# Kernel optimization log

Hardware: AMD Instinct MI355X
Metric: run time of the kernel (lower is better)

## Reference

```python
import jax, jax.numpy as jnp
import numpy as np

B, C, D, H, W = 1, 64, 24, 24, 24
N = D * H * W
K = D + H + W - 2  # cross neighbors per node (self deduped)
DS, GD = 64, 64    # d_sim, g_dim
GROUPS = C // 4
EPS = 1e-5
N_ITERS = 2        # pool_strides = [1, 1]


def _build_nbr_idx():
    i, j, k = np.meshgrid(np.arange(D), np.arange(H), np.arange(W), indexing='ij')
    i, j, k = i.reshape(-1), j.reshape(-1), k.reshape(-1)
    a0 = (j * W + k)[:, None] + np.arange(D)[None, :] * (H * W)      # (N, D) full depth line (incl self)
    full1 = (i * H * W + k)[:, None] + np.arange(H)[None, :] * W     # (N, H)
    a1 = full1[np.arange(H)[None, :] != j[:, None]].reshape(N, H - 1)
    full2 = (i * H * W + j * W)[:, None] + np.arange(W)[None, :]     # (N, W)
    a2 = full2[np.arange(W)[None, :] != k[:, None]].reshape(N, W - 1)
    return np.concatenate([a0, a1, a2], axis=1).astype(np.int32)     # (N, K)


def setup_inputs() -> dict:
    key = jax.random.key(0)
    ks = jax.random.split(key, 8)
    s = 0.05
    return {
        'x': jax.random.normal(ks[0], (B, C, D, H, W), jnp.float32),
        'nbr_idx': jnp.asarray(_build_nbr_idx()),
        'phi_w': jax.random.normal(ks[1], (DS, C), jnp.float32) * s,
        'phi_b': jnp.zeros((DS,), jnp.float32),
        'theta_w': jax.random.normal(ks[2], (DS, C), jnp.float32) * s,
        'theta_b': jnp.zeros((DS,), jnp.float32),
        'G_w': jax.random.normal(ks[3], (GD, C), jnp.float32) * s,
        'G_b': jnp.zeros((GD,), jnp.float32),
        'r_w': jax.random.normal(ks[4], (C, GD), jnp.float32) * s,
        'r_b': jnp.zeros((C,), jnp.float32),
        'gn_gamma': jnp.ones((N_ITERS, C), jnp.float32),
        'gn_beta': jnp.zeros((N_ITERS, C), jnp.float32),
        'bn_gamma': jnp.ones((C,), jnp.float32),
        'bn_beta': jnp.zeros((C,), jnp.float32),
        'bn_mean': jnp.zeros((C,), jnp.float32),
        'bn_var': jnp.ones((C,), jnp.float32),
    }


def _group_norm(v, gamma, beta):
    vg = v.reshape(B, GROUPS, C // GROUPS, D, H, W)
    m = vg.mean(axis=(2, 3, 4, 5), keepdims=True)
    var = ((vg - m) ** 2).mean(axis=(2, 3, 4, 5), keepdims=True)
    vn = ((vg - m) / jnp.sqrt(var + EPS)).reshape(B, C, D, H, W)
    return vn * gamma[None, :, None, None, None] + beta[None, :, None, None, None]


def reference(x, nbr_idx, phi_w, phi_b, theta_w, theta_b, G_w, G_b, r_w, r_b,
              gn_gamma, gn_beta, bn_gamma, bn_beta, bn_mean, bn_var):
    h = x
    for it in range(N_ITERS):
        hf = h.reshape(B, C, N).transpose(2, 0, 1)                    # (N, B, C) node features
        theta = jnp.einsum('nbc,dc->nbd', hf, theta_w) + theta_b     # (N, B, DS) queries
        phi_all = jnp.einsum('nbc,dc->nbd', hf, phi_w) + phi_b       # (N, B, DS) keys (pre-gather)
        g_all = jnp.einsum('nbc,gc->nbg', hf, G_w) + G_b             # (N, B, GD) values (pre-gather)
        phi_e = phi_all[nbr_idx]                                      # (N, K, B, DS) mailbox gather
        g_e = g_all[nbr_idx]                                          # (N, K, B, GD)
        f = jnp.einsum('nbd,nkbd->nbk', theta, phi_e)                # attention logits over K
        a = jax.nn.softmax(f, axis=-1)                                # non_local_merge 'softmax'
        y = jnp.einsum('nbk,nkbg->nbg', a, g_e)                      # weighted value sum
        cross = jnp.einsum('nbg,cg->nbc', y, r_w) + r_b              # (N, B, C) output proj
        cross = cross.transpose(1, 2, 0).reshape(B, C, D, H, W)
        h = h + _group_norm(cross, gn_gamma[it], gn_beta[it])
    # BatchNorm3d (eval, running stats) + ReLU
    bc = lambda v: v[None, :, None, None, None]
    out = (h - bc(bn_mean)) / jnp.sqrt(bc(bn_var) + EPS) * bc(bn_gamma) + bc(bn_beta)
    return jax.nn.relu(out)
```

## Files before the change

### kernel.cpp

```cpp
#include <hip/hip_runtime.h>
#include <math.h>

#define NN 13824
#define LW 24

__global__ __launch_bounds__(256) void apply_proj_kernel(
    const float* __restrict__ x,
    const float* __restrict__ cross, const float* __restrict__ gsum,
    const float* __restrict__ gn_g, const float* __restrict__ gn_b,
    float* __restrict__ h_out, int mode,
    const float* __restrict__ theta_w, const float* __restrict__ theta_b,
    const float* __restrict__ phi_w, const float* __restrict__ phi_b,
    const float* __restrict__ g_w, const float* __restrict__ g_b,
    float* __restrict__ theta, float* __restrict__ phi, float* __restrict__ gv)
{
    __shared__ float hs[64 * 64];
    __shared__ float ws[64 * 68];

    const int tid = threadIdx.x;
    const int tile = blockIdx.x / 3, ts = blockIdx.x % 3;
    const int n0 = tile * 64;

    const float* wsel = (ts == 0) ? theta_w : (ts == 1) ? phi_w : g_w;
    const float* bsel = (ts == 0) ? theta_b : (ts == 1) ? phi_b : g_b;
    float*       osel = (ts == 0) ? theta   : (ts == 1) ? phi   : gv;

    if (mode == 0) {
        for (int i = tid; i < 4096; i += 256) {
            int c = i >> 6, nl = i & 63;
            hs[c * 64 + nl] = x[(size_t)c * NN + n0 + nl];
        }
    } else {
        for (int i = tid; i < 4096; i += 256) {
            int nl = i >> 6, c = i & 63;
            ws[c * 68 + nl] = cross[(size_t)(n0 + nl) * 64 + c];
        }
        __syncthreads();
        const float inv_cnt = 1.f / 55296.f;
        for (int i = tid; i < 4096; i += 256) {
            int c = i >> 6, nl = i & 63;
            int gr = c >> 2;
            float mean = gsum[gr * 16] * inv_cnt;
            float var = gsum[512 + gr * 16] * inv_cnt - mean * mean;
            float v = (ws[c * 68 + nl] - mean) * rsqrtf(var + 1e-5f) * gn_g[c] + gn_b[c];
            size_t o = (size_t)c * NN + n0 + nl;
            float hv = x[o] + v;
            hs[c * 64 + nl] = hv;
            if (ts == 0) h_out[o] = hv;
        }
        __syncthreads();
    }

    for (int i = tid; i < 4096; i += 256) {
        int d = i >> 6, c = i & 63;
        ws[c * 68 + d] = wsel[d * 64 + c];
    }
    __syncthreads();

    const int d0  = (tid & 15) * 4;
    const int nl0 = (tid >> 4) * 4;
    float acc[4][4];
    #pragma unroll
    for (int q = 0; q < 4; q++)
        #pragma unroll
        for (int j = 0; j < 4; j++) acc[q][j] = 0.f;

    #pragma unroll 4
    for (int c = 0; c < 64; c++) {
        float4 hv = *(const float4*)&hs[c * 64 + nl0];
        float4 wv = *(const float4*)&ws[c * 68 + d0];
        #pragma unroll
        for (int j = 0; j < 4; j++) {
            float w = (&wv.x)[j];
            acc[0][j] += hv.x * w;
            acc[1][j] += hv.y * w;
            acc[2][j] += hv.z * w;
            acc[3][j] += hv.w * w;
        }
    }
    float4 bias = *(const float4*)&bsel[d0];
    #pragma unroll
    for (int q = 0; q < 4; q++) {
        float4 v;
        v.x = acc[q][0] + bias.x; v.y = acc[q][1] + bias.y;
        v.z = acc[q][2] + bias.z; v.w = acc[q][3] + bias.w;
        *(float4*)&osel[(size_t)(n0 + nl0 + q) * 64 + d0] = v;
    }
}

__global__ __launch_bounds__(128) void line_attn_kernel(
    const float* __restrict__ theta,
    const float* __restrict__ phi,
    const float* __restrict__ gv,
    float* __restrict__ y_part,
    float* __restrict__ l_part,
    float* __restrict__ gsum)
{
    __shared__ float th[2][LW * 68], ph[2][LW * 68], gs[2][LW * 68];
    __shared__ float P[2][LW * 28];

    const int tid = threadIdx.x;
    const int wv = tid >> 6, lane = tid & 63;
    const int gl = blockIdx.x * 2 + wv;
    const int axis = gl / 576, L = gl % 576;

    if (blockIdx.x == 0) {
        for (int i = tid; i < 1024; i += 128) gsum[i] = 0.f;
    }

    int base, stride;
    if (axis == 0)      { base = L * 24;                    stride = 1;   }
    else if (axis == 1) { base = (L / 24) * 576 + (L % 24); stride = 24;  }
    else                { base = L;                         stride = 576; }
    const bool excl = (axis != 2);

    #pragma unroll
    for (int q = 0; q < 6; q++) {
        int idx = q * 64 + lane;
        int row = idx >> 4, c4 = (idx & 15) * 4;
        size_t g = (size_t)(base + row * stride) * 64 + c4;
        int la = row * 68 + c4;
        *(float4*)&th[wv][la] = *(const float4*)&theta[g];
        *(float4*)&ph[wv][la] = *(const float4*)&phi[g];
        *(float4*)&gs[wv][la] = *(const float4*)&gv[g];
    }

    const int r0 = (lane >> 3) * 3, c0 = (lane & 7) * 3;
    float sa[3][3];
    #pragma unroll
    for (int a = 0; a < 3; a++)
        #pragma unroll
        for (int b = 0; b < 3; b++) sa[a][b] = 0.f;

    #pragma unroll 4
    for (int d4 = 0; d4 < 64; d4 += 4) {
        float4 t[3], p[3];
        #pragma unroll
        for (int a = 0; a < 3; a++) t[a] = *(const float4*)&th[wv][(r0 + a) * 68 + d4];
        #pragma unroll
        for (int b = 0; b < 3; b++) p[b] = *(const float4*)&ph[wv][(c0 + b) * 68 + d4];
        #pragma unroll
        for (int a = 0; a < 3; a++)
            #pragma unroll
            for (int b = 0; b < 3; b++)
                sa[a][b] += t[a].x * p[b].x + t[a].y * p[b].y +
                            t[a].z * p[b].z + t[a].w * p[b].w;
    }
    #pragma unroll
    for (int a = 0; a < 3; a++)
        #pragma unroll
        for (int b = 0; b < 3; b++) {
            float e = (excl && (r0 + a) == (c0 + b)) ? 0.f : __expf(sa[a][b]);
            P[wv][(r0 + a) * 28 + c0 + b] = e;
        }

    if (lane < 24) {
        float s = 0.f;
        #pragma unroll
        for (int c4 = 0; c4 < 24; c4 += 4) {
            float4 pv = *(const float4*)&P[wv][lane * 28 + c4];
            s += pv.x + pv.y + pv.z + pv.w;
        }
        l_part[(size_t)axis * NN + base + lane * stride] = s;
    }

    float acc[24];
    #pragma unroll
    for (int r = 0; r < 24; r++) acc[r] = 0.f;
    #pragma unroll
    for (int c4 = 0; c4 < 24; c4 += 4) {
        float g0 = gs[wv][(c4 + 0) * 68 + lane];
        float g1 = gs[wv][(c4 + 1) * 68 + lane];
        float g2 = gs[wv][(c4 + 2) * 68 + lane];
        float g3 = gs[wv][(c4 + 3) * 68 + lane];
        #pragma unroll
        for (int r = 0; r < 24; r++) {
            float4 pv = *(const float4*)&P[wv][r * 28 + c4];
            acc[r] += pv.x * g0 + pv.y * g1 + pv.z * g2 + pv.w * g3;
        }
    }
    float* yp = y_part + (size_t)axis * NN * 64;
    #pragma unroll
    for (int r = 0; r < 24; r++)
        yp[(size_t)(base + r * stride) * 64 + lane] = acc[r];
}

__global__ __launch_bounds__(256) void combine_kernel(
    const float* __restrict__ y_part, const float* __restrict__ l_part,
    const float* __restrict__ r_w, const float* __restrict__ r_b,
    float* __restrict__ cross, float* __restrict__ gsum)
{
    __shared__ float ys[16 * 68];
    __shared__ float red_s[4][64], red_ss[4][64];

    const int tid = threadIdx.x;
    const int d = tid & 63, w = tid >> 6;
    const int n0 = blockIdx.x * 16;
    const size_t S = (size_t)NN * 64;

    #pragma unroll
    for (int q = 0; q < 4; q++) {
        int nn = w * 4 + q;
        int n = n0 + nn;
        float lv = l_part[n] + l_part[NN + n] + l_part[2 * NN + n];
        size_t o = (size_t)n * 64 + d;
        float yv = y_part[o] + y_part[S + o] + y_part[2 * S + o];
        ys[nn * 68 + d] = yv / lv;
    }
    __syncthreads();

    const int c = d;
    float rb = r_b[c];
    float acc[4] = {rb, rb, rb, rb};
    for (int dd = 0; dd < 64; dd += 4) {
        float4 r4 = *(const float4*)&r_w[c * 64 + dd];
        #pragma unroll
        for (int q = 0; q < 4; q++) {
            float4 y4 = *(const float4*)&ys[(w * 4 + q) * 68 + dd];
            acc[q] += r4.x * y4.x + r4.y * y4.y + r4.z * y4.z + r4.w * y4.w;
        }
    }
    float s = 0.f, ss = 0.f;
    #pragma unroll
    for (int q = 0; q < 4; q++) {
        int n = n0 + w * 4 + q;
        cross[(size_t)n * 64 + c] = acc[q];
        s += acc[q];
        ss += acc[q] * acc[q];
    }
    red_s[w][c] = s;
    red_ss[w][c] = ss;
    __syncthreads();
    if (w == 0) {
        float ts  = red_s[0][c] + red_s[1][c] + red_s[2][c] + red_s[3][c];
        float tss = red_ss[0][c] + red_ss[1][c] + red_ss[2][c] + red_ss[3][c];
        ts  += __shfl_xor(ts, 1);  ts  += __shfl_xor(ts, 2);
        tss += __shfl_xor(tss, 1); tss += __shfl_xor(tss, 2);
        if ((c & 3) == 0) {
            atomicAdd(&gsum[(c >> 2) * 16], ts);
            atomicAdd(&gsum[512 + (c >> 2) * 16], tss);
        }
    }
}

__global__ __launch_bounds__(256) void final_kernel(
    const float* __restrict__ cross,
    const float* __restrict__ gsum,
    const float* __restrict__ gn_g, const float* __restrict__ gn_b,
    const float* __restrict__ h_in,
    const float* __restrict__ bn_g, const float* __restrict__ bn_b,
    const float* __restrict__ bn_m, const float* __restrict__ bn_v,
    float* __restrict__ out)
{
    __shared__ float t[64 * 65];
    const int tid = threadIdx.x;
    const int n0 = blockIdx.x * 64;
    for (int i = tid; i < 4096; i += 256) {
        int nl = i >> 6, c = i & 63;
        t[c * 65 + nl] = cross[(size_t)(n0 + nl) * 64 + c];
    }
    __syncthreads();
    const float inv_cnt = 1.f / 55296.f;
    for (int i = tid; i < 4096; i += 256) {
        int c = i >> 6, nl = i & 63;
        int gr = c >> 2;
        float mean = gsum[gr * 16] * inv_cnt;
        float var = gsum[512 + gr * 16] * inv_cnt - mean * mean;
        float v = (t[c * 65 + nl] - mean) * rsqrtf(var + 1e-5f) * gn_g[c] + gn_b[c];
        size_t o = (size_t)c * NN + n0 + nl;
        float h2 = h_in[o] + v;
        float bnv = (h2 - bn_m[c]) * rsqrtf(bn_v[c] + 1e-5f) * bn_g[c] + bn_b[c];
        out[o] = fmaxf(bnv, 0.f);
    }
}

extern "C" void kernel_launch(void* const* d_in, const int* in_sizes, int n_in,
                              void* d_out, int out_size, void* d_ws, size_t ws_size,
                              hipStream_t stream)
{
    const float* x        = (const float*)d_in[0];
    const float* phi_w    = (const float*)d_in[2];
    const float* phi_b    = (const float*)d_in[3];
    const float* theta_w  = (const float*)d_in[4];
    const float* theta_b  = (const float*)d_in[5];
    const float* G_w      = (const float*)d_in[6];
    const float* G_b      = (const float*)d_in[7];
    const float* r_w      = (const float*)d_in[8];
    const float* r_b      = (const float*)d_in[9];
    const float* gn_gamma = (const float*)d_in[10];
    const float* gn_beta  = (const float*)d_in[11];
    const float* bn_gamma = (const float*)d_in[12];
    const float* bn_beta  = (const float*)d_in[13];
    const float* bn_mean  = (const float*)d_in[14];
    const float* bn_var   = (const float*)d_in[15];

    float* ws = (float*)d_ws;
    const size_t S = (size_t)NN * 64;
    float* h1    = ws;
    float* theta = ws + S;
    float* phi   = ws + 2 * S;
    float* gv    = ws + 3 * S;
    float* ypart = ws + 4 * S;
    float* cross = ws + 7 * S;
    float* lpart = ws + 8 * S;
    float* gsum  = ws + 8 * S + 3 * NN;

    apply_proj_kernel<<<648, 256, 0, stream>>>(x, cross, gsum, gn_gamma, gn_beta,
                                               h1, 0,
                                               theta_w, theta_b, phi_w, phi_b,
                                               G_w, G_b, theta, phi, gv);
    line_attn_kernel<<<864, 128, 0, stream>>>(theta, phi, gv, ypart, lpart, gsum);
    combine_kernel<<<864, 256, 0, stream>>>(ypart, lpart, r_w, r_b, cross, gsum);
    apply_proj_kernel<<<648, 256, 0, stream>>>(x, cross, gsum, gn_gamma, gn_beta,
                                               h1, 1,
                                               theta_w, theta_b, phi_w, phi_b,
                                               G_w, G_b, theta, phi, gv);
    line_attn_kernel<<<864, 128, 0, stream>>>(theta, phi, gv, ypart, lpart, gsum);
    combine_kernel<<<864, 256, 0, stream>>>(ypart, lpart, r_w, r_b, cross, gsum);
    final_kernel<<<216, 256, 0, stream>>>(cross, gsum, gn_gamma + 64, gn_beta + 64,
                                          h1, bn_gamma, bn_beta, bn_mean, bn_var,
                                          (float*)d_out);
}
```

Baseline: 224.0 us.

## Fuse all stages into one persistent kernel with grid-wide barriers

Replaces the seven separate launches (projection, line attention, combine twice, then final) with one persistent kernel of 512 blocks. The blocks loop over work units in each phase and sync between phases with an atomic-counter grid barrier. This removes per-launch overhead and the idle tails between kernels. The attention phase now packs four lines per block and reads the value vectors straight from global memory instead of staging them in LDS, which frees shared memory. The risks are that all blocks must be co-resident or the barrier deadlocks, that barrier spin costs are added, and that the value reads become uncoalesced, strided global loads.

```diff
diff --git a/kernel.cpp b/kernel.cpp
--- a/kernel.cpp
+++ b/kernel.cpp
@@ -3,110 +3,130 @@
 
 #define NN 13824
 #define LW 24
-
-__global__ __launch_bounds__(256) void apply_proj_kernel(
-    const float* __restrict__ x,
-    const float* __restrict__ cross, const float* __restrict__ gsum,
-    const float* __restrict__ gn_g, const float* __restrict__ gn_b,
-    float* __restrict__ h_out, int mode,
+#define GRID 512
+#define NTHR 256
+
+__device__ __forceinline__ void gbar(unsigned* cnt, unsigned* gen)
+{
+    __syncthreads();
+    if (threadIdx.x == 0) {
+        __threadfence();
+        unsigned g = __hip_atomic_load(gen, __ATOMIC_RELAXED, __HIP_MEMORY_SCOPE_AGENT);
+        unsigned a = __hip_atomic_fetch_add(cnt, 1u, __ATOMIC_ACQ_REL, __HIP_MEMORY_SCOPE_AGENT);
+        if (a == (unsigned)gridDim.x - 1u) {
+            __hip_atomic_store(cnt, 0u, __ATOMIC_RELAXED, __HIP_MEMORY_SCOPE_AGENT);
+            __hip_atomic_store(gen, g + 1u, __ATOMIC_RELEASE, __HIP_MEMORY_SCOPE_AGENT);
+        } else {
+            while (__hip_atomic_load(gen, __ATOMIC_RELAXED, __HIP_MEMORY_SCOPE_AGENT) == g)
+                __builtin_amdgcn_s_sleep(2);
+            __builtin_amdgcn_fence(__ATOMIC_ACQUIRE, "agent");
+        }
+    }
+    __syncthreads();
+}
+
+__device__ void proj_phase(float* __restrict__ smem,
+    const float* __restrict__ x, const float* __restrict__ cross,
+    const float* __restrict__ gsum, const float* __restrict__ gn_g,
+    const float* __restrict__ gn_b, float* __restrict__ h_out, int mode,
     const float* __restrict__ theta_w, const float* __restrict__ theta_b,
     const float* __restrict__ phi_w, const float* __restrict__ phi_b,
     const float* __restrict__ g_w, const float* __restrict__ g_b,
     float* __restrict__ theta, float* __restrict__ phi, float* __restrict__ gv)
 {
-    __shared__ float hs[64 * 64];
-    __shared__ float ws[64 * 68];
-
+    float* hs = smem;
+    float* ws = smem + 4096;
     const int tid = threadIdx.x;
-    const int tile = blockIdx.x / 3, ts = blockIdx.x % 3;
-    const int n0 = tile * 64;
-
-    const float* wsel = (ts == 0) ? theta_w : (ts == 1) ? phi_w : g_w;
-    const float* bsel = (ts == 0) ? theta_b : (ts == 1) ? phi_b : g_b;
-    float*       osel = (ts == 0) ? theta   : (ts == 1) ? phi   : gv;
-
-    if (mode == 0) {
-        for (int i = tid; i < 4096; i += 256) {
-            int c = i >> 6, nl = i & 63;
-            hs[c * 64 + nl] = x[(size_t)c * NN + n0 + nl];
-        }
-    } else {
-        for (int i = tid; i < 4096; i += 256) {
-            int nl = i >> 6, c = i & 63;
-            ws[c * 68 + nl] = cross[(size_t)(n0 + nl) * 64 + c];
-        }
-        __syncthreads();
-        const float inv_cnt = 1.f / 55296.f;
-        for (int i = tid; i < 4096; i += 256) {
-            int c = i >> 6, nl = i & 63;
-            int gr = c >> 2;
-            float mean = gsum[gr * 16] * inv_cnt;
-            float var = gsum[512 + gr * 16] * inv_cnt - mean * mean;
-            float v = (ws[c * 68 + nl] - mean) * rsqrtf(var + 1e-5f) * gn_g[c] + gn_b[c];
-            size_t o = (size_t)c * NN + n0 + nl;
-            float hv = x[o] + v;
-            hs[c * 64 + nl] = hv;
-            if (ts == 0) h_out[o] = hv;
-        }
-        __syncthreads();
-    }
-
-    for (int i = tid; i < 4096; i += 256) {
-        int d = i >> 6, c = i & 63;
-        ws[c * 68 + d] = wsel[d * 64 + c];
-    }
-    __syncthreads();
-
-    const int d0  = (tid & 15) * 4;
-    const int nl0 = (tid >> 4) * 4;
-    float acc[4][4];
-    #pragma unroll
-    for (int q = 0; q < 4; q++)
-        #pragma unroll
-        for (int j = 0; j < 4; j++) acc[q][j] = 0.f;
-
-    #pragma unroll 4
-    for (int c = 0; c < 64; c++) {
-        float4 hv = *(const float4*)&hs[c * 64 + nl0];
-        float4 wv = *(const float4*)&ws[c * 68 + d0];
-        #pragma unroll
-        for (int j = 0; j < 4; j++) {
-            float w = (&wv.x)[j];
-            acc[0][j] += hv.x * w;
-            acc[1][j] += hv.y * w;
-            acc[2][j] += hv.z * w;
-            acc[3][j] += hv.w * w;
-        }
-    }
-    float4 bias = *(const float4*)&bsel[d0];
-    #pragma unroll
-    for (int q = 0; q < 4; q++) {
-        float4 v;
-        v.x = acc[q][0] + bias.x; v.y = acc[q][1] + bias.y;
-        v.z = acc[q][2] + bias.z; v.w = acc[q][3] + bias.w;
-        *(float4*)&osel[(size_t)(n0 + nl0 + q) * 64 + d0] = v;
-    }
-}
-
-__global__ __launch_bounds__(128) void line_attn_kernel(
-    const float* __restrict__ theta,
-    const float* __restrict__ phi,
-    const float* __restrict__ gv,
-    float* __restrict__ y_part,
-    float* __restrict__ l_part,
-    float* __restrict__ gsum)
-{
-    __shared__ float th[2][LW * 68], ph[2][LW * 68], gs[2][LW * 68];
-    __shared__ float P[2][LW * 28];
-
+
+    for (int unit = blockIdx.x; unit < 648; unit += GRID) {
+        const int tile = unit / 3, ts = unit % 3;
+        const int n0 = tile * 64;
+        const float* wsel = (ts == 0) ? theta_w : (ts == 1) ? phi_w : g_w;
+        const float* bsel = (ts == 0) ? theta_b : (ts == 1) ? phi_b : g_b;
+        float*       osel = (ts == 0) ? theta   : (ts == 1) ? phi   : gv;
+
+        if (mode == 0) {
+            for (int i = tid; i < 4096; i += NTHR) {
+                int c = i >> 6, nl = i & 63;
+                hs[c * 64 + nl] = x[(size_t)c * NN + n0 + nl];
+            }
+        } else {
+            for (int i = tid; i < 4096; i += NTHR) {
+                int nl = i >> 6, c = i & 63;
+                ws[c * 68 + nl] = cross[(size_t)(n0 + nl) * 64 + c];
+            }
+            __syncthreads();
+            const float inv_cnt = 1.f / 55296.f;
+            for (int i = tid; i < 4096; i += NTHR) {
+                int c = i >> 6, nl = i & 63;
+                int gr = c >> 2;
+                float mean = gsum[gr * 16] * inv_cnt;
+                float var = gsum[512 + gr * 16] * inv_cnt - mean * mean;
+                float v = (ws[c * 68 + nl] - mean) * rsqrtf(var + 1e-5f) * gn_g[c] + gn_b[c];
+                size_t o = (size_t)c * NN + n0 + nl;
+                float hv = x[o] + v;
+                hs[c * 64 + nl] = hv;
+                if (ts == 0) h_out[o] = hv;
+            }
+            __syncthreads();
+        }
+
+        for (int i = tid; i < 4096; i += NTHR) {
+            int d = i >> 6, c = i & 63;
+            ws[c * 68 + d] = wsel[d * 64 + c];
+        }
+        __syncthreads();
+
+        const int d0  = (tid & 15) * 4;
+        const int nl0 = (tid >> 4) * 4;
+        float acc[4][4];
+        #pragma unroll
+        for (int q = 0; q < 4; q++)
+            #pragma unroll
+            for (int j = 0; j < 4; j++) acc[q][j] = 0.f;
+
+        #pragma unroll 4
+        for (int c = 0; c < 64; c++) {
+            float4 hv = *(const float4*)&hs[c * 64 + nl0];
+            float4 wv = *(const float4*)&ws[c * 68 + d0];
+            #pragma unroll
+            for (int j = 0; j < 4; j++) {
+                float w = (&wv.x)[j];
+                acc[0][j] += hv.x * w;
+                acc[1][j] += hv.y * w;
+                acc[2][j] += hv.z * w;
+                acc[3][j] += hv.w * w;
+            }
+        }
+        float4 bias = *(const float4*)&bsel[d0];
+        #pragma unroll
+        for (int q = 0; q < 4; q++) {
+            float4 v;
+            v.x = acc[q][0] + bias.x; v.y = acc[q][1] + bias.y;
+            v.z = acc[q][2] + bias.z; v.w = acc[q][3] + bias.w;
+            *(float4*)&osel[(size_t)(n0 + nl0 + q) * 64 + d0] = v;
+        }
+        __syncthreads();
+    }
+}
+
+__device__ void attn_phase(float* __restrict__ smem,
+    const float* __restrict__ theta, const float* __restrict__ phi,
+    const float* __restrict__ gv, float* __restrict__ y_part,
+    float* __restrict__ l_part, float* __restrict__ gsum)
+{
     const int tid = threadIdx.x;
+    if (blockIdx.x == 0) {
+        for (int i = tid; i < 1024; i += NTHR) gsum[i] = 0.f;
+    }
     const int wv = tid >> 6, lane = tid & 63;
-    const int gl = blockIdx.x * 2 + wv;
+    const int gl = blockIdx.x * 4 + wv;
+    if (gl >= 1728) return;
     const int axis = gl / 576, L = gl % 576;
 
-    if (blockIdx.x == 0) {
-        for (int i = tid; i < 1024; i += 128) gsum[i] = 0.f;
-    }
+    float* th = smem + wv * 3936;
+    float* ph = th + 1632;
+    float* P  = th + 3264;
 
     int base, stride;
     if (axis == 0)      { base = L * 24;                    stride = 1;   }
@@ -120,9 +140,8 @@
         int row = idx >> 4, c4 = (idx & 15) * 4;
         size_t g = (size_t)(base + row * stride) * 64 + c4;
         int la = row * 68 + c4;
-        *(float4*)&th[wv][la] = *(const float4*)&theta[g];
-        *(float4*)&ph[wv][la] = *(const float4*)&phi[g];
-        *(float4*)&gs[wv][la] = *(const float4*)&gv[g];
+        *(float4*)&th[la] = *(const float4*)&theta[g];
+        *(float4*)&ph[la] = *(const float4*)&phi[g];
     }
 
     const int r0 = (lane >> 3) * 3, c0 = (lane & 7) * 3;
@@ -136,9 +155,9 @@
     for (int d4 = 0; d4 < 64; d4 += 4) {
         float4 t[3], p[3];
         #pragma unroll
-        for (int a = 0; a < 3; a++) t[a] = *(const float4*)&th[wv][(r0 + a) * 68 + d4];
-        #pragma unroll
-        for (int b = 0; b < 3; b++) p[b] = *(const float4*)&ph[wv][(c0 + b) * 68 + d4];
+        for (int a = 0; a < 3; a++) t[a] = *(const float4*)&th[(r0 + a) * 68 + d4];
+        #pragma unroll
+        for (int b = 0; b < 3; b++) p[b] = *(const float4*)&ph[(c0 + b) * 68 + d4];
         #pragma unroll
         for (int a = 0; a < 3; a++)
             #pragma unroll
@@ -151,14 +170,14 @@
         #pragma unroll
         for (int b = 0; b < 3; b++) {
             float e = (excl && (r0 + a) == (c0 + b)) ? 0.f : __expf(sa[a][b]);
-            P[wv][(r0 + a) * 28 + c0 + b] = e;
+            P[(r0 + a) * 28 + c0 + b] = e;
         }
 
     if (lane < 24) {
         float s = 0.f;
         #pragma unroll
         for (int c4 = 0; c4 < 24; c4 += 4) {
-            float4 pv = *(const float4*)&P[wv][lane * 28 + c4];
+            float4 pv = *(const float4*)&P[lane * 28 + c4];
             s += pv.x + pv.y + pv.z + pv.w;
         }
         l_part[(size_t)axis * NN + base + lane * stride] = s;
@@ -169,13 +188,13 @@
     for (int r = 0; r < 24; r++) acc[r] = 0.f;
     #pragma unroll
     for (int c4 = 0; c4 < 24; c4 += 4) {
-        float g0 = gs[wv][(c4 + 0) * 68 + lane];
-        float g1 = gs[wv][(c4 + 1) * 68 + lane];
-        float g2 = gs[wv][(c4 + 2) * 68 + lane];
-        float g3 = gs[wv][(c4 + 3) * 68 + lane];
+        float g0 = gv[(size_t)(base + (c4 + 0) * stride) * 64 + lane];
+        float g1 = gv[(size_t)(base + (c4 + 1) * stride) * 64 + lane];
+        float g2 = gv[(size_t)(base + (c4 + 2) * stride) * 64 + lane];
+        float g3 = gv[(size_t)(base + (c4 + 3) * stride) * 64 + lane];
         #pragma unroll
         for (int r = 0; r < 24; r++) {
-            float4 pv = *(const float4*)&P[wv][r * 28 + c4];
+            float4 pv = *(const float4*)&P[r * 28 + c4];
             acc[r] += pv.x * g0 + pv.y * g1 + pv.z * g2 + pv.w * g3;
         }
     }
@@ -185,93 +204,134 @@
         yp[(size_t)(base + r * stride) * 64 + lane] = acc[r];
 }
 
-__global__ __launch_bounds__(256) void combine_kernel(
+__device__ void combine_phase(float* __restrict__ smem,
     const float* __restrict__ y_part, const float* __restrict__ l_part,
     const float* __restrict__ r_w, const float* __restrict__ r_b,
     float* __restrict__ cross, float* __restrict__ gsum)
 {
-    __shared__ float ys[16 * 68];
-    __shared__ float red_s[4][64], red_ss[4][64];
-
+    float* ys = smem;
+    float* red_s = smem + 1088;
+    float* red_ss = smem + 1344;
     const int tid = threadIdx.x;
     const int d = tid & 63, w = tid >> 6;
-    const int n0 = blockIdx.x * 16;
     const size_t S = (size_t)NN * 64;
 
-    #pragma unroll
-    for (int q = 0; q < 4; q++) {
-        int nn = w * 4 + q;
-        int n = n0 + nn;
-        float lv = l_part[n] + l_part[NN + n] + l_part[2 * NN + n];
-        size_t o = (size_t)n * 64 + d;
-        float yv = y_part[o] + y_part[S + o] + y_part[2 * S + o];
-        ys[nn * 68 + d] = yv / lv;
-    }
-    __syncthreads();
-
-    const int c = d;
-    float rb = r_b[c];
-    float acc[4] = {rb, rb, rb, rb};
-    for (int dd = 0; dd < 64; dd += 4) {
-        float4 r4 = *(const float4*)&r_w[c * 64 + dd];
+    for (int u = blockIdx.x; u < 864; u += GRID) {
+        const int n0 = u * 16;
         #pragma unroll
         for (int q = 0; q < 4; q++) {
-            float4 y4 = *(const float4*)&ys[(w * 4 + q) * 68 + dd];
-            acc[q] += r4.x * y4.x + r4.y * y4.y + r4.z * y4.z + r4.w * y4.w;
-        }
-    }
-    float s = 0.f, ss = 0.f;
-    #pragma unroll
-    for (int q = 0; q < 4; q++) {
-        int n = n0 + w * 4 + q;
-        cross[(size_t)n * 64 + c] = acc[q];
-        s += acc[q];
-        ss += acc[q] * acc[q];
-    }
-    red_s[w][c] = s;
-    red_ss[w][c] = ss;
-    __syncthreads();
-    if (w == 0) {
-        float ts  = red_s[0][c] + red_s[1][c] + red_s[2][c] + red_s[3][c];
-        float tss = red_ss[0][c] + red_ss[1][c] + red_ss[2][c] + red_ss[3][c];
-        ts  += __shfl_xor(ts, 1);  ts  += __shfl_xor(ts, 2);
-        tss += __shfl_xor(tss, 1); tss += __shfl_xor(tss, 2);
-        if ((c & 3) == 0) {
-            atomicAdd(&gsum[(c >> 2) * 16], ts);
-            atomicAdd(&gsum[512 + (c >> 2) * 16], tss);
-        }
-    }
-}
-
-__global__ __launch_bounds__(256) void final_kernel(
-    const float* __restrict__ cross,
-    const float* __restrict__ gsum,
+            int nn = w * 4 + q;
+            int n = n0 + nn;
+            float lv = l_part[n] + l_part[NN + n] + l_part[2 * NN + n];
+            size_t o = (size_t)n * 64 + d;
+            float yv = y_part[o] + y_part[S + o] + y_part[2 * S + o];
+            ys[nn * 68 + d] = yv / lv;
+        }
+        __syncthreads();
+
+        const int c = d;
+        float rb = r_b[c];
+        float acc[4] = {rb, rb, rb, rb};
+        for (int dd = 0; dd < 64; dd += 4) {
+            float4 r4 = *(const float4*)&r_w[c * 64 + dd];
+            #pragma unroll
+            for (int q = 0; q < 4; q++) {
+                float4 y4 = *(const float4*)&ys[(w * 4 + q) * 68 + dd];
+                acc[q] += r4.x * y4.x + r4.y * y4.y + r4.z * y4.z + r4.w * y4.w;
+            }
+        }
+        float s = 0.f, ss = 0.f;
+        #pragma unroll
+        for (int q = 0; q < 4; q++) {
+            int n = n0 + w * 4 + q;
+            cross[(size_t)n * 64 + c] = acc[q];
+            s += acc[q];
+            ss += acc[q] * acc[q];
+        }
+        red_s[w * 64 + c] = s;
+        red_ss[w * 64 + c] = ss;
+        __syncthreads();
+        if (w == 0) {
+            float ts  = red_s[c] + red_s[64 + c] + red_s[128 + c] + red_s[192 + c];
+            float tss = red_ss[c] + red_ss[64 + c] + red_ss[128 + c] + red_ss[192 + c];
+            ts  += __shfl_xor(ts, 1);  ts  += __shfl_xor(ts, 2);
+            tss += __shfl_xor(tss, 1); tss += __shfl_xor(tss, 2);
+            if ((c & 3) == 0) {
+                atomicAdd(&gsum[(c >> 2) * 16], ts);
+                atomicAdd(&gsum[512 + (c >> 2) * 16], tss);
+            }
+        }
+        __syncthreads();
+    }
+}
+
+__device__ void final_phase(float* __restrict__ smem,
+    const float* __restrict__ cross, const float* __restrict__ gsum,
     const float* __restrict__ gn_g, const float* __restrict__ gn_b,
     const float* __restrict__ h_in,
     const float* __restrict__ bn_g, const float* __restrict__ bn_b,
     const float* __restrict__ bn_m, const float* __restrict__ bn_v,
     float* __restrict__ out)
 {
-    __shared__ float t[64 * 65];
+    float* t = smem;
     const int tid = threadIdx.x;
-    const int n0 = blockIdx.x * 64;
-    for (int i = tid; i < 4096; i += 256) {
-        int nl = i >> 6, c = i & 63;
-        t[c * 65 + nl] = cross[(size_t)(n0 + nl) * 64 + c];
-    }
-    __syncthreads();
-    const float inv_cnt = 1.f / 55296.f;
-    for (int i = tid; i < 4096; i += 256) {
-        int c = i >> 6, nl = i & 63;
-        int gr = c >> 2;
-        float mean = gsum[gr * 16] * inv_cnt;
-        float var = gsum[512 + gr * 16] * inv_cnt - mean * mean;
-        float v = (t[c * 65 + nl] - mean) * rsqrtf(var + 1e-5f) * gn_g[c] + gn_b[c];
-        size_t o = (size_t)c * NN + n0 + nl;
-        float h2 = h_in[o] + v;
-        float bnv = (h2 - bn_m[c]) * rsqrtf(bn_v[c] + 1e-5f) * bn_g[c] + bn_b[c];
-        out[o] = fmaxf(bnv, 0.f);
-    }
+    for (int u = blockIdx.x; u < 216; u += GRID) {
+        const int n0 = u * 64;
+        for (int i = tid; i < 4096; i += NTHR) {
+            int nl = i >> 6, c = i & 63;
+            t[c * 65 + nl] = cross[(size_t)(n0 + nl) * 64 + c];
+        }
+        __syncthreads();
+        const float inv_cnt = 1.f / 55296.f;
+        for (int i = tid; i < 4096; i += NTHR) {
+            int c = i >> 6, nl = i & 63;
+            int gr = c >> 2;
+            float mean = gsum[gr * 16] * inv_cnt;
+            float var = gsum[512 + gr * 16] * inv_cnt - mean * mean;
+            float v = (t[c * 65 + nl] - mean) * rsqrtf(var + 1e-5f) * gn_g[c] + gn_b[c];
+            size_t o = (size_t)c * NN + n0 + nl;
+            float h2 = h_in[o] + v;
+            float bnv = (h2 - bn_m[c]) * rsqrtf(bn_v[c] + 1e-5f) * bn_g[c] + bn_b[c];
+            out[o] = fmaxf(bnv, 0.f);
+        }
+        __syncthreads();
+    }
+}
+
+__global__ __launch_bounds__(NTHR, 2) void fused_all(
+    const float* __restrict__ x,
+    const float* __restrict__ theta_w, const float* __restrict__ theta_b,
+    const float* __restrict__ phi_w, const float* __restrict__ phi_b,
+    const float* __restrict__ G_w, const float* __restrict__ G_b,
+    const float* __restrict__ r_w, const float* __restrict__ r_b,
+    const float* __restrict__ gn_gamma, const float* __restrict__ gn_beta,
+    const float* __restrict__ bn_g, const float* __restrict__ bn_b,
+    const float* __restrict__ bn_m, const float* __restrict__ bn_v,
+    float* __restrict__ h1, float* __restrict__ theta, float* __restrict__ phi,
+    float* __restrict__ gv, float* __restrict__ ypart, float* __restrict__ cross,
+    float* __restrict__ lpart, float* __restrict__ gsum,
+    unsigned* __restrict__ bar, float* __restrict__ out)
+{
+    __shared__ float smem[15744];
+    unsigned* cnt = bar;
+    unsigned* gen = bar + 32;
+
+    proj_phase(smem, x, cross, gsum, gn_gamma, gn_beta, h1, 0,
+               theta_w, theta_b, phi_w, phi_b, G_w, G_b, theta, phi, gv);
+    gbar(cnt, gen);
+    attn_phase(smem, theta, phi, gv, ypart, lpart, gsum);
+    gbar(cnt, gen);
+    combine_phase(smem, ypart, lpart, r_w, r_b, cross, gsum);
+    gbar(cnt, gen);
+    proj_phase(smem, x, cross, gsum, gn_gamma, gn_beta, h1, 1,
+               theta_w, theta_b, phi_w, phi_b, G_w, G_b, theta, phi, gv);
+    gbar(cnt, gen);
+    attn_phase(smem, theta, phi, gv, ypart, lpart, gsum);
+    gbar(cnt, gen);
+    combine_phase(smem, ypart, lpart, r_w, r_b, cross, gsum);
+    gbar(cnt, gen);
+    final_phase(smem, cross, gsum, gn_gamma + 64, gn_beta + 64, h1,
+                bn_g, bn_b, bn_m, bn_v, out);
 }
 
 extern "C" void kernel_launch(void* const* d_in, const int* in_sizes, int n_in,
@@ -304,20 +364,12 @@
     float* cross = ws + 7 * S;
     float* lpart = ws + 8 * S;
     float* gsum  = ws + 8 * S + 3 * NN;
-
-    apply_proj_kernel<<<648, 256, 0, stream>>>(x, cross, gsum, gn_gamma, gn_beta,
-                                               h1, 0,
-                                               theta_w, theta_b, phi_w, phi_b,
-                                               G_w, G_b, theta, phi, gv);
-    line_attn_kernel<<<864, 128, 0, stream>>>(theta, phi, gv, ypart, lpart, gsum);
-    combine_kernel<<<864, 256, 0, stream>>>(ypart, lpart, r_w, r_b, cross, gsum);
-    apply_proj_kernel<<<648, 256, 0, stream>>>(x, cross, gsum, gn_gamma, gn_beta,
-                                               h1, 1,
-                                               theta_w, theta_b, phi_w, phi_b,
-                                               G_w, G_b, theta, phi, gv);
-    line_attn_kernel<<<864, 128, 0, stream>>>(theta, phi, gv, ypart, lpart, gsum);
-    combine_kernel<<<864, 256, 0, stream>>>(ypart, lpart, r_w, r_b, cross, gsum);
-    final_kernel<<<216, 256, 0, stream>>>(cross, gsum, gn_gamma + 64, gn_beta + 64,
-                                          h1, bn_gamma, bn_beta, bn_mean, bn_var,
-                                          (float*)d_out);
-}
+    unsigned* bar = (unsigned*)(ws + 8 * S + 3 * NN + 1024);
+
+    hipMemsetAsync(bar, 0, 256, stream);
+
+    fused_all<<<GRID, NTHR, 0, stream>>>(
+        x, theta_w, theta_b, phi_w, phi_b, G_w, G_b, r_w, r_b,
+        gn_gamma, gn_beta, bn_gamma, bn_beta, bn_mean, bn_var,
+        h1, theta, phi, gv, ypart, cross, lpart, gsum, bar, (float*)d_out);
+}
```

New measurement: 385.7 us. +72.2%, slower.
